# Kernel tuning notes

Measured on AMD Instinct MI355X. Metric: run time of the kernel, lower is better.

The kernel has to match this reference:

```python
import jax, jax.numpy as jnp
import numpy as np

EPS = 0.05    # geomloss: blur**p with p=1, blur=0.05
NITER = 30    # fixed Sinkhorn iterations (geomloss uses eps-scaling; fixed-eps loop is the reference math)


def _cost(x, y):
    # x:(N,3), y:(M,3) -> (N,M) Euclidean distance (p=1 ground cost)
    d2 = jnp.sum((x[:, None, :] - y[None, :, :]) ** 2, axis=-1)
    return jnp.sqrt(d2 + 1e-12)


def _sinkhorn_ot(x, y):
    # Entropic OT cost between uniform measures on x (N pts) and y (M pts), log-domain Sinkhorn.
    n, m = x.shape[0], y.shape[0]
    C = _cost(x, y)                                  # (N,M)
    log_a = jnp.full((n,), -jnp.log(jnp.float32(n)), dtype=x.dtype)
    log_b = jnp.full((m,), -jnp.log(jnp.float32(m)), dtype=x.dtype)

    def step(carry, _):
        f, g = carry
        # f_i = -eps * LSE_j( log_b_j + (g_j - C_ij)/eps )
        f = -EPS * jax.nn.logsumexp(log_b[None, :] + (g[None, :] - C) / EPS, axis=1)
        g = -EPS * jax.nn.logsumexp(log_a[:, None] + (f[:, None] - C) / EPS, axis=0)
        return (f, g), None

    f0 = jnp.zeros((n,), dtype=x.dtype)
    g0 = jnp.zeros((m,), dtype=x.dtype)
    (f, g), _ = jax.lax.scan(step, (f0, g0), None, length=NITER)
    a = jnp.exp(log_a)
    b = jnp.exp(log_b)
    return jnp.sum(a * f) + jnp.sum(b * g)


def _sinkhorn_divergence(x, y):
    # Debiased Sinkhorn divergence: S(x,y) = OT(x,y) - 0.5*OT(x,x) - 0.5*OT(y,y)
    return _sinkhorn_ot(x, y) - 0.5 * _sinkhorn_ot(x, x) - 0.5 * _sinkhorn_ot(y, y)


def setup_inputs() -> dict:
    key = jax.random.key(0)
    k1, k2 = jax.random.split(key)
    B, N, M = 8, 2048, 2048
    xyz1 = jax.random.normal(k1, (B, N, 3), dtype=jnp.float32)
    xyz2 = jax.random.normal(k2, (B, M, 3), dtype=jnp.float32)
    return {"xyz1": xyz1, "xyz2": xyz2}


def reference(xyz1, xyz2):
    # Per-batch Sinkhorn divergence, averaged over batch (original loops over b; vmap is the
    # vectorized equivalent since clouds are independent).
    losses = jax.vmap(_sinkhorn_divergence)(xyz1, xyz2)   # (B,)
    return jnp.sum(losses) / xyz1.shape[0]
```

## Files before the change

### kernel.cpp

```cpp
#include <hip/hip_runtime.h>

#define NPTS    2048
#define NBATCH  8
#define NPROB   24
#define NITER   30
#define TPB     512
#define WPB     8
#define NJOBS   32
#define HCOLS   1024

constexpr float KSC = 28.853900817779268f;
constexpr float C1f = 0.38123094930796995f;
constexpr float C2f = 0.03465735902799726f;

typedef float v2f __attribute__((ext_vector_type(2)));

__device__ __forceinline__ float fexp2(float x) { return __builtin_amdgcn_exp2f(x); }
__device__ __forceinline__ float flog2(float x) { return __builtin_amdgcn_logf(x); }
__device__ __forceinline__ float fsqrt(float x) { return __builtin_amdgcn_sqrtf(x); }

__device__ __forceinline__ unsigned long long mspread(unsigned v) {
    unsigned long long x = v & 1023ull;
    x = (x | (x << 16)) & 0x030000FFull;
    x = (x | (x << 8))  & 0x0300F00Full;
    x = (x | (x << 4))  & 0x030C30C3ull;
    x = (x | (x << 2))  & 0x09249249ull;
    return x;
}
__device__ __forceinline__ unsigned q10(float v) {
    int q = (int)((v + 8.0f) * 64.0f);
    return (unsigned)(q < 0 ? 0 : (q > 1023 ? 1023 : q));
}

__global__ __launch_bounds__(TPB)
void prep_sort(const float* __restrict__ xyz1, const float* __restrict__ xyz2,
               float* __restrict__ pc, float* __restrict__ bbox)
{
    __shared__ unsigned long long keys[NPTS];
    const int s  = blockIdx.x;
    const int b  = s >> 1;
    const float* src = (s & 1) ? (xyz2 + (size_t)b * NPTS * 3)
                               : (xyz1 + (size_t)b * NPTS * 3);
    const int tid = threadIdx.x;

    for (int i = tid; i < NPTS; i += TPB) {
        float x = src[3*i], y = src[3*i+1], z = src[3*i+2];
        unsigned long long code = (mspread(q10(x)) << 2) |
                                  (mspread(q10(y)) << 1) |
                                   mspread(q10(z));
        keys[i] = (code << 11) | (unsigned long long)i;
    }
    __syncthreads();

    for (int k = 2; k <= NPTS; k <<= 1) {
        for (int j = k >> 1; j > 0; j >>= 1) {
            for (int t = tid; t < NPTS / 2; t += TPB) {
                const int lo = t & (j - 1);
                const int i  = ((t - lo) << 1) + lo;
                const int ix = i + j;
                const bool asc = ((i & k) == 0);
                unsigned long long a = keys[i], c = keys[ix];
                if ((a > c) == asc) { keys[i] = c; keys[ix] = a; }
            }
            __syncthreads();
        }
    }

    float* dst = pc + (size_t)s * NPTS * 3;
    for (int i = tid; i < NPTS; i += TPB) {
        const int pi = (int)(keys[i] & 2047ull);
        dst[3*i+0] = src[3*pi+0];
        dst[3*i+1] = src[3*pi+1];
        dst[3*i+2] = src[3*pi+2];
    }

    if (tid < 32) {
        float lox = 1e30f, loy = 1e30f, loz = 1e30f;
        float hix = -1e30f, hiy = -1e30f, hiz = -1e30f;
        for (int q = 0; q < 64; ++q) {
            const int pi = (int)(keys[tid * 64 + q] & 2047ull);
            const float x = src[3*pi], y = src[3*pi+1], z = src[3*pi+2];
            lox = fminf(lox, x); hix = fmaxf(hix, x);
            loy = fminf(loy, y); hiy = fmaxf(hiy, y);
            loz = fminf(loz, z); hiz = fmaxf(hiz, z);
        }
        float* bb = bbox + ((size_t)s * 32 + tid) * 8;
        bb[0] = lox; bb[1] = loy; bb[2] = loz;
        bb[3] = hix; bb[4] = hiy; bb[5] = hiz;
        bb[6] = 0.f; bb[7] = 0.f;
    }
}

__global__ __launch_bounds__(256)
void init_sums(float* __restrict__ gsum)
{
    int i = blockIdx.x * 256 + threadIdx.x;
    if (i < NPROB * 2 * NPTS) gsum[i] = 1024.0f;
}

__device__ __forceinline__ void problem_barrier(unsigned* arrive, unsigned* epoch,
                                                unsigned phase, int nbpp, int tid)
{
    __syncthreads();
    if (tid == 0) {
        unsigned old = __hip_atomic_fetch_add(arrive, 1u, __ATOMIC_ACQ_REL,
                                              __HIP_MEMORY_SCOPE_AGENT);
        if (old == (unsigned)(nbpp - 1)) {
            __hip_atomic_store(arrive, 0u, __ATOMIC_RELAXED, __HIP_MEMORY_SCOPE_AGENT);
            __hip_atomic_store(epoch, phase, __ATOMIC_RELEASE, __HIP_MEMORY_SCOPE_AGENT);
        } else {
            while (__hip_atomic_load(epoch, __ATOMIC_RELAXED,
                                     __HIP_MEMORY_SCOPE_AGENT) < phase) {
                __builtin_amdgcn_s_sleep(2);
            }
            __threadfence();
        }
    }
    __syncthreads();
}

__global__ __launch_bounds__(TPB, 6)
void sinkhorn_all(const float* __restrict__ pc,
                  float* __restrict__ fsum,
                  float* __restrict__ gsum,
                  unsigned* __restrict__ bars,
                  int nbpp)
{
    __shared__ float4 shC[2][HCOLS];
    __shared__ float  shS[WPB][128];

    const int tid  = threadIdx.x;
    const int lane = tid & 63;
    const int warp = tid >> 6;
    const int p    = blockIdx.x % NPROB;
    const int lb   = blockIdx.x / NPROB;
    const int b    = p / 3;
    const int k    = p - 3 * b;

    const float* xb = pc + (size_t)(2 * b) * NPTS * 3;
    const float* yb = pc + (size_t)(2 * b + 1) * NPTS * 3;
    float* fS = fsum + (size_t)p * 2 * NPTS;
    float* gS = gsum + (size_t)p * 2 * NPTS;
    unsigned* arrive = bars + (size_t)p * 64;
    unsigned* epoch  = bars + (size_t)p * 64 + 32;

    const float* Uf = (k == 2) ? yb : xb;
    const float* Ug = (k == 0) ? yb : ((k == 1) ? xb : yb);
    const float* Vf = (k == 1) ? xb : yb;
    const float* Vg = (k == 2) ? yb : xb;
    const int sideG = (Vg == Vf) ? 0 : 1;

    auto stage_coords = [&](const float* __restrict__ V, int side, int h) {
        if (tid < 256) {
            const float4* V4 = (const float4*)V;
            const int i0 = 3 * (h * 256 + tid);
            const float4 a  = V4[i0 + 0];
            const float4 bb = V4[i0 + 1];
            const float4 cc = V4[i0 + 2];
            const int c = 4 * tid;
            shC[side][c + 0] = make_float4(a.x,  a.y,  a.z,  0.f);
            shC[side][c + 1] = make_float4(a.w,  bb.x, bb.y, 0.f);
            shC[side][c + 2] = make_float4(bb.z, bb.w, cc.x, 0.f);
            shC[side][c + 3] = make_float4(cc.y, cc.z, cc.w, 0.f);
        }
    };
    auto stage_w = [&](const float* __restrict__ S, int side, int h) {
        const int c  = 2 * tid;
        const int gc = h * HCOLS + c;
        const float2 t0 = *(const float2*)(S + gc);
        const float2 t1 = *(const float2*)(S + NPTS + gc);
        shC[side][c + 0].w = 11.0f - flog2(t0.x + t1.x);
        shC[side][c + 1].w = 11.0f - flog2(t0.y + t1.y);
    };
    auto stage_full = [&](const float* __restrict__ V, const float* __restrict__ S,
                          int side, int h) {
        if (tid < 256) {
            const float4* V4 = (const float4*)V;
            const int i0 = 3 * (h * 256 + tid);
            const float4 a  = V4[i0 + 0];
            const float4 bb = V4[i0 + 1];
            const float4 cc = V4[i0 + 2];
            const int c  = 4 * tid;
            const int gc = h * HCOLS + c;
            const float4 t0 = *(const float4*)(S + gc);
            const float4 t1 = *(const float4*)(S + NPTS + gc);
            shC[side][c + 0] = make_float4(a.x,  a.y,  a.z,  11.0f - flog2(t0.x + t1.x));
            shC[side][c + 1] = make_float4(a.w,  bb.x, bb.y, 11.0f - flog2(t0.y + t1.y));
            shC[side][c + 2] = make_float4(bb.z, bb.w, cc.x, 11.0f - flog2(t0.z + t1.z));
            shC[side][c + 3] = make_float4(cc.y, cc.z, cc.w, 11.0f - flog2(t0.w + t1.w));
        }
    };

    auto do_pass = [&](const float* __restrict__ U, float* __restrict__ oS,
                       int side, int h, int rc) {
        __syncthreads();
        const int r0 = rc * 128 + lane, r1 = r0 + 64;
        const v2f ux = {U[3*r0],   U[3*r1]};
        const v2f uy = {U[3*r0+1], U[3*r1+1]};
        const v2f uz = {U[3*r0+2], U[3*r1+2]};
        const v2f e12 = {1e-12f, 1e-12f};
        const v2f nK  = {-KSC, -KSC};
        v2f s0 = {0.f, 0.f}, s1 = {0.f, 0.f}, s2 = {0.f, 0.f}, s3 = {0.f, 0.f};

        auto term = [&](const float4 v) -> v2f {
            v2f dx = ux - (v2f){v.x, v.x};
            v2f dy = uy - (v2f){v.y, v.y};
            v2f dz = uz - (v2f){v.z, v.z};
            v2f d2 = __builtin_elementwise_fma(dz, dz, e12);
            d2 = __builtin_elementwise_fma(dy, dy, d2);
            d2 = __builtin_elementwise_fma(dx, dx, d2);
            v2f sq  = {fsqrt(d2.x), fsqrt(d2.y)};
            v2f arg = __builtin_elementwise_fma(nK, sq, (v2f){v.w, v.w});
            return (v2f){fexp2(arg.x), fexp2(arg.y)};
        };
        const int cbase = warp * 4;
        #pragma unroll 2
        for (int g = 0; g < 32; ++g) {
            const int c = cbase + g * 32;
            const float4 v0 = shC[side][c + 0];
            const float4 v1 = shC[side][c + 1];
            const float4 v2 = shC[side][c + 2];
            const float4 v3 = shC[side][c + 3];
            s0 += term(v0);
            s1 += term(v1);
            s2 += term(v2);
            s3 += term(v3);
        }
        shS[warp][lane]      = (s0.x + s1.x) + (s2.x + s3.x);
        shS[warp][lane + 64] = (s0.y + s1.y) + (s2.y + s3.y);
        __syncthreads();
        if (tid < 128) {
            float t = shS[0][tid];
            #pragma unroll
            for (int w = 1; w < WPB; ++w) t += shS[w][tid];
            oS[h * NPTS + rc * 128 + tid] = t;
        }
        __syncthreads();
    };

    if (nbpp == NJOBS) {
        const int h  = lb & 1;
        const int rc = lb >> 1;
        stage_coords(Vf, 0, h);
        if (sideG == 1) stage_coords(Vg, 1, h);

        for (int it = 0; it < NITER; ++it) {
            stage_w(gS, 0, h);
            do_pass(Uf, fS, 0, h, rc);
            problem_barrier(arrive, epoch, (unsigned)(2 * it + 1), nbpp, tid);
            stage_w(fS, sideG, h);
            do_pass(Ug, gS, sideG, h, rc);
            problem_barrier(arrive, epoch, (unsigned)(2 * it + 2), nbpp, tid);
        }
    } else {
        for (int it = 0; it < NITER; ++it) {
            for (int j = lb; j < NJOBS; j += nbpp) {
                stage_full(Vf, gS, 0, j & 1);
                do_pass(Uf, fS, 0, j & 1, j >> 1);
            }
            problem_barrier(arrive, epoch, (unsigned)(2 * it + 1), nbpp, tid);
            for (int j = lb; j < NJOBS; j += nbpp) {
                stage_full(Vg, fS, 0, j & 1);
                do_pass(Ug, gS, 0, j & 1, j >> 1);
            }
            problem_barrier(arrive, epoch, (unsigned)(2 * it + 2), nbpp, tid);
        }
    }
}

__global__ __launch_bounds__(TPB, 1)
void final_reduce(const float* __restrict__ fsum, const float* __restrict__ gsum,
                  float* __restrict__ out)
{
    __shared__ double red[WPB];
    const int tid  = threadIdx.x;
    const int lane = tid & 63;
    const int warp = tid >> 6;

    double acc = 0.0;
    for (int idx = tid; idx < 2 * NPROB * NPTS; idx += TPB) {
        const bool isF = idx < NPROB * NPTS;
        const int rem  = isF ? idx : idx - NPROB * NPTS;
        const int pp   = rem >> 11;
        const int j    = rem & (NPTS - 1);
        const float* S = (isF ? fsum : gsum) + (size_t)pp * 2 * NPTS;
        const float t  = S[j] + S[NPTS + j];
        const float val = C1f - C2f * flog2(t);
        const float w   = (pp % 3 == 0) ? 1.0f : -0.5f;
        acc += (double)val * (double)w;
    }
    #pragma unroll
    for (int off = 32; off > 0; off >>= 1) acc += __shfl_xor(acc, off);
    if (lane == 0) red[warp] = acc;
    __syncthreads();
    if (warp == 0) {
        double v2 = (lane < WPB) ? red[lane] : 0.0;
        #pragma unroll
        for (int off = 32; off > 0; off >>= 1) v2 += __shfl_xor(v2, off);
        if (lane == 0) out[0] = (float)(v2 / (double)(NBATCH * NPTS));
    }
}

extern "C" void kernel_launch(void* const* d_in, const int* in_sizes, int n_in,
                              void* d_out, int out_size, void* d_ws, size_t ws_size,
                              hipStream_t stream)
{
    const float* xyz1 = (const float*)d_in[0];
    const float* xyz2 = (const float*)d_in[1];
    float* out = (float*)d_out;

    float* fsum = (float*)d_ws;
    float* gsum = fsum + (size_t)NPROB * 2 * NPTS;
    float* pc   = gsum + (size_t)NPROB * 2 * NPTS;
    float* bbox = pc   + (size_t)16 * NPTS * 3;
    unsigned* bars = (unsigned*)(bbox + (size_t)16 * 32 * 8);

    hipMemsetAsync(bars, 0, (size_t)NPROB * 64 * sizeof(unsigned), stream);
    prep_sort<<<16, TPB, 0, stream>>>(xyz1, xyz2, pc, bbox);
    init_sums<<<(NPROB * 2 * NPTS + 255) / 256, 256, 0, stream>>>(gsum);

    int maxB = 0;
    hipOccupancyMaxActiveBlocksPerMultiprocessor(&maxB, sinkhorn_all, TPB, 0);
    if (maxB < 1) maxB = 1;
    int bpp = (maxB * 256) / NPROB;
    if (bpp > NJOBS) bpp = NJOBS;
    if (bpp < 1) bpp = 1;
    int nblk = NPROB * bpp;

    void* args[] = { (void*)&pc, (void*)&fsum, (void*)&gsum, (void*)&bars, (void*)&bpp };
    hipLaunchCooperativeKernel((void*)sinkhorn_all, dim3(nblk), dim3(TPB),
                               args, 0, stream);

    final_reduce<<<1, TPB, 0, stream>>>(fsum, gsum, out);
}
```

Baseline: 2.554 ms.

## Skip negligible column tiles using bounding-box bounds in Sinkhorn passes

Uses the per-tile bounding boxes from the Morton sort, together with the per-tile min and max of the dual weights, to compute a lower bound on each row's log-sum-exp. Any 64-column tile whose best possible contribution falls more than a fixed margin below that bound is skipped for the whole warp. This cuts sqrt/exp work in the full-occupancy path. The cost is extra bound computation, warp-wide shuffle reductions while staging weights, and branch divergence. Accuracy depends on the margin, because contributions below it are dropped.

Result: no change. 2.556 ms (+0.1%).

```diff
diff --git a/kernel.cpp b/kernel.cpp
--- a/kernel.cpp
+++ b/kernel.cpp
@@ -8,10 +8,13 @@
 #define WPB     8
 #define NJOBS   32
 #define HCOLS   1024
-
-constexpr float KSC = 28.853900817779268f;
-constexpr float C1f = 0.38123094930796995f;
-constexpr float C2f = 0.03465735902799726f;
+#define NTIL    16
+#define MARGIN  28.0f
+
+constexpr float KSC  = 28.853900817779268f;
+constexpr float INVK = 0.034657359027997264f;
+constexpr float C1f  = 0.38123094930796995f;
+constexpr float C2f  = 0.03465735902799726f;
 
 typedef float v2f __attribute__((ext_vector_type(2)));
 
@@ -85,9 +88,8 @@
             loz = fminf(loz, z); hiz = fmaxf(hiz, z);
         }
         float* bb = bbox + ((size_t)s * 32 + tid) * 8;
-        bb[0] = lox; bb[1] = loy; bb[2] = loz;
-        bb[3] = hix; bb[4] = hiy; bb[5] = hiz;
-        bb[6] = 0.f; bb[7] = 0.f;
+        bb[0] = lox; bb[1] = loy; bb[2] = loz; bb[3] = hix;
+        bb[4] = hiy; bb[5] = hiz; bb[6] = 0.f; bb[7] = 0.f;
     }
 }
 
@@ -121,6 +123,7 @@
 
 __global__ __launch_bounds__(TPB, 6)
 void sinkhorn_all(const float* __restrict__ pc,
+                  const float* __restrict__ bbox,
                   float* __restrict__ fsum,
                   float* __restrict__ gsum,
                   unsigned* __restrict__ bars,
@@ -128,6 +131,9 @@
 {
     __shared__ float4 shC[2][HCOLS];
     __shared__ float  shS[WPB][128];
+    __shared__ float4 shB[2][NTIL][2];
+    __shared__ float  shTmax[NTIL];
+    __shared__ float  shTmin[NTIL];
 
     const int tid  = threadIdx.x;
     const int lane = tid & 63;
@@ -149,6 +155,8 @@
     const float* Vf = (k == 1) ? xb : yb;
     const float* Vg = (k == 2) ? yb : xb;
     const int sideG = (Vg == Vf) ? 0 : 1;
+    const int sVf   = 2 * b + ((k == 1) ? 0 : 1);
+    const int sVg   = 2 * b + ((k == 2) ? 1 : 0);
 
     auto stage_coords = [&](const float* __restrict__ V, int side, int h) {
         if (tid < 256) {
@@ -169,8 +177,20 @@
         const int gc = h * HCOLS + c;
         const float2 t0 = *(const float2*)(S + gc);
         const float2 t1 = *(const float2*)(S + NPTS + gc);
-        shC[side][c + 0].w = 11.0f - flog2(t0.x + t1.x);
-        shC[side][c + 1].w = 11.0f - flog2(t0.y + t1.y);
+        const float w0 = 11.0f - flog2(t0.x + t1.x);
+        const float w1 = 11.0f - flog2(t0.y + t1.y);
+        shC[side][c + 0].w = w0;
+        shC[side][c + 1].w = w1;
+        float wmx = fmaxf(w0, w1), wmn = fminf(w0, w1);
+        #pragma unroll
+        for (int m = 1; m < 32; m <<= 1) {
+            wmx = fmaxf(wmx, __shfl_xor(wmx, m));
+            wmn = fminf(wmn, __shfl_xor(wmn, m));
+        }
+        if ((tid & 31) == 0) {
+            shTmax[tid >> 5] = wmx;
+            shTmin[tid >> 5] = wmn;
+        }
     };
     auto stage_full = [&](const float* __restrict__ V, const float* __restrict__ S,
                           int side, int h) {
@@ -192,7 +212,7 @@
     };
 
     auto do_pass = [&](const float* __restrict__ U, float* __restrict__ oS,
-                       int side, int h, int rc) {
+                       int side, int h, int rc, bool trunc) {
         __syncthreads();
         const int r0 = rc * 128 + lane, r1 = r0 + 64;
         const v2f ux = {U[3*r0],   U[3*r1]};
@@ -201,6 +221,56 @@
         const v2f e12 = {1e-12f, 1e-12f};
         const v2f nK  = {-KSC, -KSC};
         v2f s0 = {0.f, 0.f}, s1 = {0.f, 0.f}, s2 = {0.f, 0.f}, s3 = {0.f, 0.f};
+
+        unsigned mask = 0xFFFFu;
+        if (trunc) {
+            float LB0 = -3.0e38f, LB1 = -3.0e38f;
+            #pragma unroll 4
+            for (int t = 0; t < NTIL; ++t) {
+                const float4 A = shB[side][t][0];
+                const float4 B = shB[side][t][1];
+                const float wmn = shTmin[t];
+                {
+                    const float ex = fmaxf(ux.x - A.x, A.w - ux.x);
+                    const float ey = fmaxf(uy.x - A.y, B.x - uy.x);
+                    const float ez = fmaxf(uz.x - A.z, B.y - uz.x);
+                    const float dmx = fsqrt(fmaf(ex, ex, fmaf(ey, ey, ez * ez)));
+                    LB0 = fmaxf(LB0, fmaf(-KSC, dmx, wmn));
+                }
+                {
+                    const float ex = fmaxf(ux.y - A.x, A.w - ux.y);
+                    const float ey = fmaxf(uy.y - A.y, B.x - uy.y);
+                    const float ez = fmaxf(uz.y - A.z, B.y - uz.y);
+                    const float dmx = fsqrt(fmaf(ex, ex, fmaf(ey, ey, ez * ez)));
+                    LB1 = fmaxf(LB1, fmaf(-KSC, dmx, wmn));
+                }
+            }
+            mask = 0;
+            #pragma unroll 4
+            for (int t = 0; t < NTIL; ++t) {
+                const float4 A = shB[side][t][0];
+                const float4 B = shB[side][t][1];
+                const float wmx = shTmax[t];
+                bool sk0, sk1;
+                {
+                    const float ex = fmaxf(fmaxf(A.x - ux.x, ux.x - A.w), 0.f);
+                    const float ey = fmaxf(fmaxf(A.y - uy.x, uy.x - B.x), 0.f);
+                    const float ez = fmaxf(fmaxf(A.z - uz.x, uz.x - B.y), 0.f);
+                    const float dmin2 = fmaf(ex, ex, fmaf(ey, ey, ez * ez));
+                    const float rhs = fmaxf(wmx - LB0 + MARGIN, 0.f) * INVK;
+                    sk0 = dmin2 > rhs * rhs;
+                }
+                {
+                    const float ex = fmaxf(fmaxf(A.x - ux.y, ux.y - A.w), 0.f);
+                    const float ey = fmaxf(fmaxf(A.y - uy.y, uy.y - B.x), 0.f);
+                    const float ez = fmaxf(fmaxf(A.z - uz.y, uz.y - B.y), 0.f);
+                    const float dmin2 = fmaf(ex, ex, fmaf(ey, ey, ez * ez));
+                    const float rhs = fmaxf(wmx - LB1 + MARGIN, 0.f) * INVK;
+                    sk1 = dmin2 > rhs * rhs;
+                }
+                if (__any(!(sk0 && sk1))) mask |= (1u << t);
+            }
+        }
 
         auto term = [&](const float4 v) -> v2f {
             v2f dx = ux - (v2f){v.x, v.x};
@@ -214,17 +284,24 @@
             return (v2f){fexp2(arg.x), fexp2(arg.y)};
         };
         const int cbase = warp * 4;
-        #pragma unroll 2
-        for (int g = 0; g < 32; ++g) {
-            const int c = cbase + g * 32;
-            const float4 v0 = shC[side][c + 0];
-            const float4 v1 = shC[side][c + 1];
-            const float4 v2 = shC[side][c + 2];
-            const float4 v3 = shC[side][c + 3];
-            s0 += term(v0);
-            s1 += term(v1);
-            s2 += term(v2);
-            s3 += term(v3);
+        for (int t = 0; t < NTIL; ++t) {
+            if (!((mask >> t) & 1u)) continue;
+            const int cA = 64 * t + cbase;
+            {
+                const float4 v0 = shC[side][cA + 0];
+                const float4 v1 = shC[side][cA + 1];
+                const float4 v2 = shC[side][cA + 2];
+                const float4 v3 = shC[side][cA + 3];
+                s0 += term(v0); s1 += term(v1); s2 += term(v2); s3 += term(v3);
+            }
+            {
+                const int cB = cA + 32;
+                const float4 v0 = shC[side][cB + 0];
+                const float4 v1 = shC[side][cB + 1];
+                const float4 v2 = shC[side][cB + 2];
+                const float4 v3 = shC[side][cB + 3];
+                s0 += term(v0); s1 += term(v1); s2 += term(v2); s3 += term(v3);
+            }
         }
         shS[warp][lane]      = (s0.x + s1.x) + (s2.x + s3.x);
         shS[warp][lane + 64] = (s0.y + s1.y) + (s2.y + s3.y);
@@ -243,25 +320,35 @@
         const int rc = lb >> 1;
         stage_coords(Vf, 0, h);
         if (sideG == 1) stage_coords(Vg, 1, h);
+        if (tid < NTIL) {
+            const float* bb = bbox + ((size_t)sVf * 32 + h * NTIL + tid) * 8;
+            shB[0][tid][0] = make_float4(bb[0], bb[1], bb[2], bb[3]);
+            shB[0][tid][1] = make_float4(bb[4], bb[5], 0.f, 0.f);
+        } else if (tid < 2 * NTIL) {
+            const int t = tid - NTIL;
+            const float* bb = bbox + ((size_t)sVg * 32 + h * NTIL + t) * 8;
+            shB[1][t][0] = make_float4(bb[0], bb[1], bb[2], bb[3]);
+            shB[1][t][1] = make_float4(bb[4], bb[5], 0.f, 0.f);
+        }
 
         for (int it = 0; it < NITER; ++it) {
             stage_w(gS, 0, h);
-            do_pass(Uf, fS, 0, h, rc);
+            do_pass(Uf, fS, 0, h, rc, true);
             problem_barrier(arrive, epoch, (unsigned)(2 * it + 1), nbpp, tid);
             stage_w(fS, sideG, h);
-            do_pass(Ug, gS, sideG, h, rc);
+            do_pass(Ug, gS, sideG, h, rc, true);
             problem_barrier(arrive, epoch, (unsigned)(2 * it + 2), nbpp, tid);
         }
     } else {
         for (int it = 0; it < NITER; ++it) {
             for (int j = lb; j < NJOBS; j += nbpp) {
                 stage_full(Vf, gS, 0, j & 1);
-                do_pass(Uf, fS, 0, j & 1, j >> 1);
+                do_pass(Uf, fS, 0, j & 1, j >> 1, false);
             }
             problem_barrier(arrive, epoch, (unsigned)(2 * it + 1), nbpp, tid);
             for (int j = lb; j < NJOBS; j += nbpp) {
                 stage_full(Vg, fS, 0, j & 1);
-                do_pass(Ug, gS, 0, j & 1, j >> 1);
+                do_pass(Ug, gS, 0, j & 1, j >> 1, false);
             }
             problem_barrier(arrive, epoch, (unsigned)(2 * it + 2), nbpp, tid);
         }
@@ -327,7 +414,8 @@
     if (bpp < 1) bpp = 1;
     int nblk = NPROB * bpp;
 
-    void* args[] = { (void*)&pc, (void*)&fsum, (void*)&gsum, (void*)&bars, (void*)&bpp };
+    void* args[] = { (void*)&pc, (void*)&bbox, (void*)&fsum, (void*)&gsum,
+                     (void*)&bars, (void*)&bpp };
     hipLaunchCooperativeKernel((void*)sinkhorn_all, dim3(nblk), dim3(TPB),
                                args, 0, stream);
 
```
